# Kernel optimization log

Measured on AMD Instinct MI355X. Metric: run time of the kernel, lower is better.

Reference implementation:

```python
import jax, jax.numpy as jnp
import numpy as np

HEADS = 16
WINDOW = 256
D_MODEL = 1024


def _ln(x, g, b, eps=1e-5):
    m = jnp.mean(x, -1, keepdims=True)
    var = jnp.mean((x - m) ** 2, -1, keepdims=True)
    return (x - m) * jax.lax.rsqrt(var + eps) * g + b


def _proj(x, g, b, W, bias):
    # torch: nn.Sequential(LayerNorm(d), Linear(d, h))
    return _ln(x, g, b) @ W.T + bias


def _bucket(x, pad_value):
    # x: (..., L, d) -> (..., nb, window, d), seq padded to multiple of window with pad_value
    L = x.shape[-2]
    n = WINDOW * (-(-L // WINDOW))
    pads = [(0, 0)] * x.ndim
    pads[-2] = (0, n - L)
    x = jnp.pad(x, pads, constant_values=pad_value)
    return x.reshape(*x.shape[:-2], n // WINDOW, WINDOW, x.shape[-1])


def _unfold(x, pad_value):
    # x: (..., nb, w, d) -> (..., nb, 2w, d): previous bucket (pad_value for bucket 0) || current
    pads = [(0, 0)] * x.ndim
    pads[-3] = (1, 0)
    prev = jnp.pad(x, pads, constant_values=pad_value)[..., :-1, :, :]
    return jnp.concatenate([prev, x], axis=-2)


def _rotary(x):
    # lucidrains rotary_embedding_torch default: theta=10000, interleaved pairs, positions 0..S-1 along dim -2
    S, d = x.shape[-2], x.shape[-1]
    inv = 1.0 / (10000.0 ** (jnp.arange(0, d, 2, dtype=jnp.float32) / d))
    freqs = jnp.arange(S, dtype=jnp.float32)[:, None] * inv[None, :]  # (S, d/2)
    freqs = jnp.repeat(freqs, 2, axis=-1)  # (S, d)
    cos, sin = jnp.cos(freqs).astype(x.dtype), jnp.sin(freqs).astype(x.dtype)
    xp = x.reshape(*x.shape[:-1], d // 2, 2)
    xr = jnp.stack([-xp[..., 1], xp[..., 0]], axis=-1).reshape(x.shape)
    return x * cos + xr * sin


def _forward(q, k, v, cell,
             ln_q_w, ln_q_b, w_q, b_q,
             ln_k_w, ln_k_b, w_k, b_k,
             ln_v_w, ln_v_b, w_v, b_v,
             ln_o_w, ln_o_b, w_o, b_o):
    B, L, D = q.shape
    hd = D // HEADS

    def split_heads(x):  # (B, L, D) -> (B, H, L, hd)
        return x.reshape(B, L, HEADS, hd).transpose(0, 2, 1, 3)

    qh = split_heads(_proj(q, ln_q_w, ln_q_b, w_q, b_q))
    kh = split_heads(_proj(k, ln_k_w, ln_k_b, w_k, b_k))
    vh = split_heads(_proj(v, ln_v_w, ln_v_b, w_v, b_v))

    bq = _bucket(qh, -1.0)                 # (B, H, nb, w, hd)
    bk = _unfold(_bucket(kh, -1.0), -1.0)  # (B, H, nb, 2w, hd)
    bv = _unfold(_bucket(vh, -1.0), -1.0)

    nb = bq.shape[2]
    n = nb * WINDOW
    i = _bucket(jnp.arange(n, dtype=jnp.int32)[:, None], -1)   # (nb, w, 1)
    j = jnp.swapaxes(_unfold(i, -1), -1, -2)                    # (nb, 1, 2w)
    mask = (i >= j) & (j != -1)                                 # (nb, w, 2w) causal + left pad
    req = _bucket(cell, -1)                                     # (B, 1, nb, w, 1)
    rek = jnp.swapaxes(_unfold(req, -1), -1, -2)                # (B, 1, nb, 1, 2w)
    mask = mask & (req == rek)                                  # (B, 1, nb, w, 2w)

    bq = _rotary(bq)
    bk = _rotary(bk)

    p = jnp.einsum('bhnqd,bhnkd->bhnqk', bq, bk) / jnp.sqrt(jnp.asarray(hd, bq.dtype))
    p = jnp.where(mask, p, jnp.finfo(p.dtype).min)
    a = jax.nn.softmax(p, axis=-1)
    o = jnp.einsum('bhnqk,bhnkd->bhnqd', a, bv)   # (B, H, nb, w, hd)
    o = o.reshape(B, HEADS, n, hd)[:, :, :L]      # drop seq padding
    o = o.transpose(0, 2, 1, 3).reshape(B, L, D)  # merge heads
    return _proj(o, ln_o_w, ln_o_b, w_o, b_o)


def setup_inputs() -> dict:
    key = jax.random.key(0)
    ks = jax.random.split(key, 10)
    B, L, D = 2, 4096, D_MODEL
    inp = {
        'q': jax.random.normal(ks[0], (B, L, D), dtype=jnp.float32),
        'k': jax.random.normal(ks[1], (B, L, D), dtype=jnp.float32),
        'v': jax.random.normal(ks[2], (B, L, D), dtype=jnp.float32),
        'cell': jnp.sort(jax.random.randint(ks[3], (B, 1, L, 1), 0, 64, dtype=jnp.int32), axis=2),
    }
    for idx, name in enumerate(['q', 'k', 'v', 'o']):
        inp[f'ln_{name}_w'] = jnp.ones((D,), jnp.float32)
        inp[f'ln_{name}_b'] = jnp.zeros((D,), jnp.float32)
        inp[f'w_{name}'] = jax.random.normal(ks[4 + idx], (D, D), dtype=jnp.float32) * 0.02
        inp[f'b_{name}'] = jnp.zeros((D,), jnp.float32)
    return inp


def reference(q, k, v, cell,
              ln_q_w, ln_q_b, w_q, b_q,
              ln_k_w, ln_k_b, w_k, b_k,
              ln_v_w, ln_v_b, w_v, b_v,
              ln_o_w, ln_o_b, w_o, b_o):
    return _forward(q, k, v, cell,
                    ln_q_w, ln_q_b, w_q, b_q,
                    ln_k_w, ln_k_b, w_k, b_k,
                    ln_v_w, ln_v_b, w_v, b_v,
                    ln_o_w, ln_o_b, w_o, b_o)
```

## Files before the change

### kernel.cpp

```cpp
#include <hip/hip_runtime.h>

#define HEADS 16
#define HD 64
#define DM 1024
#define LSEQ 4096
#define NEGF (-1.0e30f)

typedef __attribute__((ext_vector_type(8))) short bf16x8;
typedef __attribute__((ext_vector_type(4))) float f32x4;
typedef unsigned short u16;

#define MFMA16(a, b, c) __builtin_amdgcn_mfma_f32_16x16x32_bf16((a), (b), (c), 0, 0, 0)

static __device__ __forceinline__ float b2f(u16 u) {
  union { float f; unsigned i; } t; t.i = ((unsigned)u) << 16; return t.f;
}
static __device__ __forceinline__ u16 f2b(float f) {
  union { float f; unsigned i; } t; t.f = f;
  unsigned r = t.i + 0x7fffu + ((t.i >> 16) & 1u);
  return (u16)(r >> 16);
}
static __device__ __forceinline__ ushort4 pk4(float4 v) {
  return make_ushort4(f2b(v.x), f2b(v.y), f2b(v.z), f2b(v.w));
}
static __device__ __forceinline__ void gload16(const void* g, void* l) {
  __builtin_amdgcn_global_load_lds((const __attribute__((address_space(1))) void*)g,
                                   (__attribute__((address_space(3))) void*)l, 16, 0, 0);
}

__global__ void rope_build(float* __restrict__ ropc, float* __restrict__ rops) {
  int p = blockIdx.x, d = threadIdx.x;
  int t2 = d & ~1;
  double inv = pow(10000.0, -(double)t2 / 64.0);
  double f = (double)p * inv;
  ropc[p * 64 + d] = (float)cos(f);
  rops[p * 64 + d] = (float)sin(f);
}

__global__ void cvtw(const float4* __restrict__ a, const float4* __restrict__ b,
                     const float4* __restrict__ c, const float4* __restrict__ d,
                     ushort4* __restrict__ out) {
  int i = blockIdx.x * blockDim.x + threadIdx.x;
  out[i]          = pk4(a[i]);
  out[i + 262144] = pk4(b[i]);
  out[i + 524288] = pk4(c[i]);
  out[i + 786432] = pk4(d[i]);
}

__global__ __launch_bounds__(256) void ln_qkv(
    const float4* __restrict__ q, const float4* __restrict__ k, const float4* __restrict__ v,
    const float* __restrict__ g0, const float* __restrict__ b0,
    const float* __restrict__ g1, const float* __restrict__ b1,
    const float* __restrict__ g2, const float* __restrict__ b2,
    ushort4* __restrict__ o0, ushort4* __restrict__ o1, ushort4* __restrict__ o2) {
  const int row = blockIdx.x, tid = threadIdx.x, sel = blockIdx.y;
  const float4* src = (sel == 0) ? q : (sel == 1) ? k : v;
  const float* gam = (sel == 0) ? g0 : (sel == 1) ? g1 : g2;
  const float* bet = (sel == 0) ? b0 : (sel == 1) ? b1 : b2;
  ushort4* dst = (sel == 0) ? o0 : (sel == 1) ? o1 : o2;

  float4 v4 = src[(size_t)row * 256 + tid];
  float s = v4.x + v4.y + v4.z + v4.w;
  float s2 = v4.x * v4.x + v4.y * v4.y + v4.z * v4.z + v4.w * v4.w;
#pragma unroll
  for (int d = 1; d < 64; d <<= 1) { s += __shfl_xor(s, d); s2 += __shfl_xor(s2, d); }
  __shared__ float ps[8];
  int lane = tid & 63, wave = tid >> 6;
  if (lane == 0) { ps[wave] = s; ps[4 + wave] = s2; }
  __syncthreads();
  float tot = ps[0] + ps[1] + ps[2] + ps[3];
  float tot2 = ps[4] + ps[5] + ps[6] + ps[7];
  float mean = tot * (1.f / 1024.f);
  float var = tot2 * (1.f / 1024.f) - mean * mean;
  float rstd = rsqrtf(var + 1e-5f);
  float4 gv = ((const float4*)gam)[tid];
  float4 bv = ((const float4*)bet)[tid];
  dst[(size_t)row * 256 + tid] = make_ushort4(
      f2b((v4.x - mean) * rstd * gv.x + bv.x), f2b((v4.y - mean) * rstd * gv.y + bv.y),
      f2b((v4.z - mean) * rstd * gv.z + bv.z), f2b((v4.w - mean) * rstd * gv.w + bv.w));
}

__global__ __launch_bounds__(256) void ln_rows(const ushort4* __restrict__ xin,
                                               const float* __restrict__ gam,
                                               const float* __restrict__ bet,
                                               ushort4* __restrict__ out) {
  int row = blockIdx.x, tid = threadIdx.x;
  ushort4 u = xin[(size_t)row * 256 + tid];
  float4 v;
  v.x = b2f(u.x); v.y = b2f(u.y); v.z = b2f(u.z); v.w = b2f(u.w);
  float s = v.x + v.y + v.z + v.w;
  float s2 = v.x * v.x + v.y * v.y + v.z * v.z + v.w * v.w;
#pragma unroll
  for (int d = 1; d < 64; d <<= 1) { s += __shfl_xor(s, d); s2 += __shfl_xor(s2, d); }
  __shared__ float ps[8];
  int lane = tid & 63, wave = tid >> 6;
  if (lane == 0) { ps[wave] = s; ps[4 + wave] = s2; }
  __syncthreads();
  float tot = ps[0] + ps[1] + ps[2] + ps[3];
  float tot2 = ps[4] + ps[5] + ps[6] + ps[7];
  float mean = tot * (1.f / 1024.f);
  float var = tot2 * (1.f / 1024.f) - mean * mean;
  float rstd = rsqrtf(var + 1e-5f);
  float4 gv = ((const float4*)gam)[tid];
  float4 bv = ((const float4*)bet)[tid];
  out[(size_t)row * 256 + tid] = make_ushort4(
      f2b((v.x - mean) * rstd * gv.x + bv.x), f2b((v.y - mean) * rstd * gv.y + bv.y),
      f2b((v.z - mean) * rstd * gv.z + bv.z), f2b((v.w - mean) * rstd * gv.w + bv.w));
}

__global__ __launch_bounds__(256, 3) void gemm_qkv(
    const u16* __restrict__ Aq, const u16* __restrict__ Ak, const u16* __restrict__ Av,
    const u16* __restrict__ wbf,
    const float* __restrict__ bq, const float* __restrict__ bk, const float* __restrict__ bv,
    const float* __restrict__ ropc, const float* __restrict__ rops,
    u16* __restrict__ qrot, u16* __restrict__ krA, u16* __restrict__ krB,
    u16* __restrict__ vTp) {
  __shared__ __align__(16) u16 Als[128 * 64];
  __shared__ __align__(16) u16 Bls[128 * 64];
  const int tid = threadIdx.x, lane = tid & 63, wave = tid >> 6;
  const int g = lane >> 4, ln15 = lane & 15;
  const int mode = blockIdx.y;
  const u16* A = (mode == 0) ? Aq : (mode == 1) ? Ak : Av;
  const u16* Bw = wbf + (size_t)mode * 1048576;
  const float* bias = (mode == 0) ? bq : (mode == 1) ? bk : bv;
  const int bid = blockIdx.x;
  const int xcd = bid & 7, idx = bid >> 3;
  const int row0 = (xcd * 8 + (idx >> 3)) * 128;
  const int col0 = (idx & 7) * 128;
  const int wm = (wave >> 1) * 64, wn = (wave & 1) * 64;
  const int K = 1024;
  f32x4 acc[4][4] = {};

  for (int k0 = 0; k0 < K; k0 += 64) {
#pragma unroll
    for (int i = 0; i < 4; ++i) {
      int ch = i * 4 + wave;
      int olin = ch * 1024 + lane * 16;
      int r = olin >> 7;
      int cel = ((olin ^ ((r & 7) << 4)) >> 1) & 63;
      gload16(A + (size_t)(row0 + r) * K + k0 + cel, (char*)Als + ch * 1024);
    }
#pragma unroll
    for (int i = 0; i < 4; ++i) {
      int ch = i * 4 + wave;
      int olin = ch * 1024 + lane * 16;
      int r = olin >> 7;
      int cel = ((olin ^ ((r & 7) << 4)) >> 1) & 63;
      gload16(Bw + (size_t)(col0 + r) * K + k0 + cel, (char*)Bls + ch * 1024);
    }
    __syncthreads();
#pragma unroll
    for (int ks = 0; ks < 2; ++ks) {
      bf16x8 af[4], bfv[4];
      int cb = (ks * 32 + g * 8) * 2;
#pragma unroll
      for (int mi = 0; mi < 4; ++mi) {
        int r = wm + mi * 16 + ln15;
        af[mi] = *(const bf16x8*)((const char*)Als + r * 128 + (cb ^ ((r & 7) << 4)));
      }
#pragma unroll
      for (int ni = 0; ni < 4; ++ni) {
        int r = wn + ni * 16 + ln15;
        bfv[ni] = *(const bf16x8*)((const char*)Bls + r * 128 + (cb ^ ((r & 7) << 4)));
      }
#pragma unroll
      for (int mi = 0; mi < 4; ++mi)
#pragma unroll
        for (int ni = 0; ni < 4; ++ni)
          acc[mi][ni] = MFMA16(af[mi], bfv[ni], acc[mi][ni]);
    }
    __syncthreads();
  }

#pragma unroll
  for (int mi = 0; mi < 4; ++mi)
#pragma unroll
    for (int ni = 0; ni < 4; ++ni)
#pragma unroll
      for (int r = 0; r < 4; ++r) {
        int row = row0 + wm + mi * 16 + g * 4 + r;
        int col = col0 + wn + ni * 16 + ln15;
        float val = acc[mi][ni][r] + bias[col];
        int bb = row >> 12, l = row & 4095, hh = col >> 6, d = col & 63;
        if (mode == 2) {
          vTp[(((size_t)bb * HEADS + hh) * HD + d) * LSEQ + l] = f2b(val);
        } else {
          if (mode == 0) val *= 0.125f;
          float oth = __shfl_xor(val, 1);
          int pB = l & 255;
          size_t oidx = (((size_t)bb * HEADS + hh) * LSEQ + l) * HD + d;
          if (mode == 0) {
            float cc = ropc[pB * 64 + d], ss = rops[pB * 64 + d];
            qrot[oidx] = f2b((d & 1) ? (val * cc + oth * ss) : (val * cc - oth * ss));
          } else {
            int pA = 256 + pB;
            float cA = ropc[pA * 64 + d], sA = rops[pA * 64 + d];
            krA[oidx] = f2b((d & 1) ? (val * cA + oth * sA) : (val * cA - oth * sA));
            float cB = ropc[pB * 64 + d], sB = rops[pB * 64 + d];
            krB[oidx] = f2b((d & 1) ? (val * cB + oth * sB) : (val * cB - oth * sB));
          }
        }
      }
}

__global__ __launch_bounds__(256, 3) void gemm_o(
    const u16* __restrict__ A, const u16* __restrict__ Bw, const float* __restrict__ bias,
    float* __restrict__ outf) {
  __shared__ __align__(16) u16 Als[128 * 64];
  __shared__ __align__(16) u16 Bls[128 * 64];
  const int tid = threadIdx.x, lane = tid & 63, wave = tid >> 6;
  const int g = lane >> 4, ln15 = lane & 15;
  const int bid = blockIdx.x;
  const int xcd = bid & 7, idx = bid >> 3;
  const int row0 = (xcd * 8 + (idx >> 3)) * 128;
  const int col0 = (idx & 7) * 128;
  const int wm = (wave >> 1) * 64, wn = (wave & 1) * 64;
  const int K = 1024, N = 1024;
  f32x4 acc[4][4] = {};

  for (int k0 = 0; k0 < K; k0 += 64) {
#pragma unroll
    for (int i = 0; i < 4; ++i) {
      int ch = i * 4 + wave;
      int olin = ch * 1024 + lane * 16;
      int r = olin >> 7;
      int cel = ((olin ^ ((r & 7) << 4)) >> 1) & 63;
      gload16(A + (size_t)(row0 + r) * K + k0 + cel, (char*)Als + ch * 1024);
    }
#pragma unroll
    for (int i = 0; i < 4; ++i) {
      int ch = i * 4 + wave;
      int olin = ch * 1024 + lane * 16;
      int r = olin >> 7;
      int cel = ((olin ^ ((r & 7) << 4)) >> 1) & 63;
      gload16(Bw + (size_t)(col0 + r) * K + k0 + cel, (char*)Bls + ch * 1024);
    }
    __syncthreads();
#pragma unroll
    for (int ks = 0; ks < 2; ++ks) {
      bf16x8 af[4], bfv[4];
      int cb = (ks * 32 + g * 8) * 2;
#pragma unroll
      for (int mi = 0; mi < 4; ++mi) {
        int r = wm + mi * 16 + ln15;
        af[mi] = *(const bf16x8*)((const char*)Als + r * 128 + (cb ^ ((r & 7) << 4)));
      }
#pragma unroll
      for (int ni = 0; ni < 4; ++ni) {
        int r = wn + ni * 16 + ln15;
        bfv[ni] = *(const bf16x8*)((const char*)Bls + r * 128 + (cb ^ ((r & 7) << 4)));
      }
#pragma unroll
      for (int mi = 0; mi < 4; ++mi)
#pragma unroll
        for (int ni = 0; ni < 4; ++ni)
          acc[mi][ni] = MFMA16(af[mi], bfv[ni], acc[mi][ni]);
    }
    __syncthreads();
  }

#pragma unroll
  for (int mi = 0; mi < 4; ++mi)
#pragma unroll
    for (int ni = 0; ni < 4; ++ni)
#pragma unroll
      for (int r = 0; r < 4; ++r) {
        int row = row0 + wm + mi * 16 + g * 4 + r;
        int col = col0 + wn + ni * 16 + ln15;
        outf[(size_t)row * N + col] = acc[mi][ni][r] + bias[col];
      }
}

__global__ __launch_bounds__(512, 2) void attn_kernel(
    const u16* __restrict__ qrot,
    const u16* __restrict__ krotA,
    const u16* __restrict__ krotB,
    const u16* __restrict__ vT,
    const int* __restrict__ cell,
    u16* __restrict__ o) {
  __shared__ __align__(16) u16 Kc[2][128 * 64];
  __shared__ __align__(16) u16 Pl[8 * 32 * 64];
  __shared__ int ci[256];
  __shared__ int cj[512];

  const int tid = threadIdx.x, lane = tid & 63, wave = tid >> 6;
  const int g = lane >> 4, ln15 = lane & 15;
  const int bucket = blockIdx.x & 15;
  const int h = (blockIdx.x >> 4) & 15;
  const int b = blockIdx.x >> 8;
  const int w0 = bucket * 256;
  const size_t base = (size_t)(b * HEADS + h) * LSEQ * HD;

  if (tid < 256) ci[tid] = cell[b * LSEQ + w0 + tid];
  {
    int gj = w0 - 256 + tid;
    cj[tid] = (gj >= 0) ? cell[b * LSEQ + gj] : (int)0x80000000;
  }

  bf16x8 qf[2][2];
#pragma unroll
  for (int mi = 0; mi < 2; ++mi)
#pragma unroll
    for (int ks = 0; ks < 2; ++ks)
      qf[mi][ks] = *(const bf16x8*)(qrot + base +
          (size_t)(w0 + wave * 32 + mi * 16 + ln15) * HD + ks * 32 + g * 8);

  f32x4 Oa[2][4] = {};
  float mrow[2][4], lrow[2][4];
#pragma unroll
  for (int a1 = 0; a1 < 2; ++a1)
#pragma unroll
    for (int a2 = 0; a2 < 4; ++a2) { mrow[a1][a2] = NEGF; lrow[a1][a2] = 0.f; }

#define STAGE_K(bi, s)                                                          \
  {                                                                             \
    const u16* ksrc_ = ((s) < 2) ? krotB : krotA;                               \
    int gj0_ = w0 - 256 + (s) * 128;                                            \
    _Pragma("unroll")                                                           \
    for (int i_ = 0; i_ < 2; ++i_) {                                            \
      int ch_ = i_ * 8 + wave;                                                  \
      int olin_ = ch_ * 1024 + lane * 16;                                       \
      int r_ = olin_ >> 7;                                                      \
      int cel_ = ((olin_ ^ ((r_ & 7) << 4)) >> 1) & 63;                         \
      gload16(ksrc_ + base + (size_t)(gj0_ + r_) * HD + cel_,                   \
              (char*)Kc[bi] + ch_ * 1024);                                      \
    }                                                                           \
  }

  const int s0 = (bucket == 0) ? 2 : 0;
  STAGE_K(0, s0);
  __syncthreads();

  const int crb_lo = ci[0], crb_hi = ci[255];
  const int crw_lo = ci[wave * 32], crw_hi = ci[wave * 32 + 31];

  for (int s = s0; s < 4; ++s) {
    const int cur = (s - s0) & 1;
    if (s + 1 < 4) {
      int k1 = (s + 1) * 2;
      bool need = false;
#pragma unroll
      for (int kk = 0; kk < 2; ++kk) {
        int clo = cj[(k1 + kk) * 64], chi = cj[(k1 + kk) * 64 + 63];
        need = need || !(chi < crb_lo || clo > crb_hi);
      }
      if (need) STAGE_K(cur ^ 1, s + 1);
    }

#pragma unroll
    for (int sub = 0; sub < 2; ++sub) {
      const int k = s * 2 + sub;
      if (k * 64 > wave * 32 + 287) continue;
      {
        int clo = cj[k * 64], chi = cj[k * 64 + 63];
        if (chi < crw_lo || clo > crw_hi) continue;
      }
      const int gj0 = w0 - 256 + k * 64;
      const int lr0 = sub * 64;

#pragma unroll
      for (int mi = 0; mi < 2; ++mi) {
        f32x4 sc[4] = {};
        __builtin_amdgcn_s_setprio(1);
#pragma unroll
        for (int ks = 0; ks < 2; ++ks) {
          int cb = (ks * 32 + g * 8) * 2;
#pragma unroll
          for (int ni = 0; ni < 4; ++ni) {
            int r = lr0 + ni * 16 + ln15;
            bf16x8 kf = *(const bf16x8*)((const char*)Kc[cur] + r * 128 + (cb ^ ((r & 7) << 4)));
            sc[ni] = MFMA16(qf[mi][ks], kf, sc[ni]);
          }
        }
        __builtin_amdgcn_s_setprio(0);
        float mx[4] = {NEGF, NEGF, NEGF, NEGF};
#pragma unroll
        for (int ni = 0; ni < 4; ++ni)
#pragma unroll
          for (int r = 0; r < 4; ++r) {
            int iloc = wave * 32 + mi * 16 + g * 4 + r;
            int p = k * 64 + ni * 16 + ln15;
            bool ok = (p <= iloc + 256) && (ci[iloc] == cj[p]);
            float sv = ok ? sc[ni][r] : NEGF;
            sc[ni][r] = sv;
            mx[r] = fmaxf(mx[r], sv);
          }
#pragma unroll
        for (int d = 1; d < 16; d <<= 1)
#pragma unroll
          for (int r = 0; r < 4; ++r) mx[r] = fmaxf(mx[r], __shfl_xor(mx[r], d));
        float rs[4] = {0.f, 0.f, 0.f, 0.f};
        bool big = false;
#pragma unroll
        for (int r = 0; r < 4; ++r) big = big || (mx[r] > mrow[mi][r] + 8.0f);
        if (__any(big)) {
#pragma unroll
          for (int r = 0; r < 4; ++r) {
            float mold = mrow[mi][r];
            float mnew = fmaxf(mold, mx[r]);
            float alpha = __expf(mold - mnew);
            mrow[mi][r] = mnew;
            lrow[mi][r] *= alpha;
#pragma unroll
            for (int nd = 0; nd < 4; ++nd) Oa[mi][nd][r] *= alpha;
          }
        }
#pragma unroll
        for (int ni = 0; ni < 4; ++ni)
#pragma unroll
          for (int r = 0; r < 4; ++r) {
            float sv = sc[ni][r];
            float p = (sv > NEGF * 0.5f) ? __expf(sv - mrow[mi][r]) : 0.f;
            rs[r] += p;
            int row = mi * 16 + g * 4 + r;
            int colb = (ni * 16 + ln15) * 2;
            *(u16*)((char*)Pl + wave * 4096 + row * 128 + (colb ^ ((row & 7) << 4))) = f2b(p);
          }
#pragma unroll
        for (int d = 1; d < 16; d <<= 1)
#pragma unroll
          for (int r = 0; r < 4; ++r) rs[r] += __shfl_xor(rs[r], d);
#pragma unroll
        for (int r = 0; r < 4; ++r) lrow[mi][r] += rs[r];
      }

#pragma unroll
      for (int jb = 0; jb < 2; ++jb) {
        bf16x8 pa[2], vb[4];
        int cb = (jb * 32 + g * 8) * 2;
#pragma unroll
        for (int mi = 0; mi < 2; ++mi) {
          int row = mi * 16 + ln15;
          pa[mi] = *(const bf16x8*)((const char*)Pl + wave * 4096 + row * 128 + (cb ^ ((row & 7) << 4)));
        }
#pragma unroll
        for (int nd = 0; nd < 4; ++nd) {
          int d = nd * 16 + ln15;
          int p0 = gj0 + jb * 32 + g * 8;
          vb[nd] = *(const bf16x8*)(vT + base + (size_t)d * LSEQ + p0);
        }
        __builtin_amdgcn_s_setprio(1);
#pragma unroll
        for (int mi = 0; mi < 2; ++mi)
#pragma unroll
          for (int nd = 0; nd < 4; ++nd) Oa[mi][nd] = MFMA16(pa[mi], vb[nd], Oa[mi][nd]);
        __builtin_amdgcn_s_setprio(0);
      }
    }

    __syncthreads();
  }

#pragma unroll
  for (int mi = 0; mi < 2; ++mi)
#pragma unroll
    for (int r = 0; r < 4; ++r) {
      float invl = 1.0f / lrow[mi][r];
      int gi = w0 + wave * 32 + mi * 16 + g * 4 + r;
      size_t ob = ((size_t)b * LSEQ + gi) * DM + h * HD;
#pragma unroll
      for (int nd = 0; nd < 4; ++nd) o[ob + nd * 16 + ln15] = f2b(Oa[mi][nd][r] * invl);
    }
#undef STAGE_K
}

extern "C" void kernel_launch(void* const* d_in, const int* in_sizes, int n_in,
                              void* d_out, int out_size, void* d_ws, size_t ws_size,
                              hipStream_t stream) {
  const float* q = (const float*)d_in[0];
  const float* k = (const float*)d_in[1];
  const float* v = (const float*)d_in[2];
  const int* cell = (const int*)d_in[3];
  const float* lnw[4] = {(const float*)d_in[4], (const float*)d_in[8], (const float*)d_in[12], (const float*)d_in[16]};
  const float* lnb[4] = {(const float*)d_in[5], (const float*)d_in[9], (const float*)d_in[13], (const float*)d_in[17]};
  const float* Wm[4]  = {(const float*)d_in[6], (const float*)d_in[10], (const float*)d_in[14], (const float*)d_in[18]};
  const float* bi[4]  = {(const float*)d_in[7], (const float*)d_in[11], (const float*)d_in[15], (const float*)d_in[19]};

  char* ws = (char*)d_ws;
  u16* xlnq  = (u16*)(ws);
  u16* wbf   = (u16*)(ws + 16777216);
  u16* qrot  = (u16*)(ws + 25165824);
  u16* krA   = (u16*)(ws + 41943040);
  u16* krB   = (u16*)(ws + 58720256);
  u16* vT    = (u16*)(ws + 75497472);
  u16* obuf  = (u16*)(ws + 92274688);
  float* ropc = (float*)(ws + 109051904);
  float* rops = (float*)(ws + 109182976);
  u16* xlnk = obuf;
  u16* xlnv = (u16*)d_out;

  cvtw<<<1024, 256, 0, stream>>>((const float4*)Wm[0], (const float4*)Wm[1],
                                 (const float4*)Wm[2], (const float4*)Wm[3], (ushort4*)wbf);
  rope_build<<<512, 64, 0, stream>>>(ropc, rops);

  dim3 lng(8192, 3);
  ln_qkv<<<lng, 256, 0, stream>>>((const float4*)q, (const float4*)k, (const float4*)v,
                                  lnw[0], lnb[0], lnw[1], lnb[1], lnw[2], lnb[2],
                                  (ushort4*)xlnq, (ushort4*)xlnk, (ushort4*)xlnv);
  dim3 gq(512, 3);
  gemm_qkv<<<gq, 256, 0, stream>>>(xlnq, xlnk, xlnv, wbf, bi[0], bi[1], bi[2],
                                   ropc, rops, qrot, krA, krB, vT);
  attn_kernel<<<512, 512, 0, stream>>>(qrot, krA, krB, vT, cell, obuf);
  ln_rows<<<8192, 256, 0, stream>>>((const ushort4*)obuf, lnw[3], lnb[3], (ushort4*)xlnq);
  gemm_o<<<512, 256, 0, stream>>>(xlnq, wbf + 3145728, bi[3], (float*)d_out);
}
```

Baseline: 214.7 us.

## Stage QKV GEMM epilogue through LDS and drop duplicate rotated K buffer

```diff
diff --git a/kernel.cpp b/kernel.cpp
--- a/kernel.cpp
+++ b/kernel.cpp
@@ -113,10 +113,10 @@
     const u16* __restrict__ wbf,
     const float* __restrict__ bq, const float* __restrict__ bk, const float* __restrict__ bv,
     const float* __restrict__ ropc, const float* __restrict__ rops,
-    u16* __restrict__ qrot, u16* __restrict__ krA, u16* __restrict__ krB,
-    u16* __restrict__ vTp) {
-  __shared__ __align__(16) u16 Als[128 * 64];
-  __shared__ __align__(16) u16 Bls[128 * 64];
+    u16* __restrict__ qrot, u16* __restrict__ krot, u16* __restrict__ vTp) {
+  __shared__ __align__(16) char smem[34816];
+  u16* Als = (u16*)smem;
+  u16* Bls = (u16*)(smem + 16384);
   const int tid = threadIdx.x, lane = tid & 63, wave = tid >> 6;
   const int g = lane >> 4, ln15 = lane & 15;
   const int mode = blockIdx.y;
@@ -172,35 +172,51 @@
     __syncthreads();
   }
 
+  u16* Cl = (u16*)smem;
 #pragma unroll
   for (int mi = 0; mi < 4; ++mi)
 #pragma unroll
     for (int ni = 0; ni < 4; ++ni)
 #pragma unroll
       for (int r = 0; r < 4; ++r) {
-        int row = row0 + wm + mi * 16 + g * 4 + r;
-        int col = col0 + wn + ni * 16 + ln15;
+        int rowc = wm + mi * 16 + g * 4 + r;
+        int colc = wn + ni * 16 + ln15;
+        int row = row0 + rowc, col = col0 + colc;
         float val = acc[mi][ni][r] + bias[col];
-        int bb = row >> 12, l = row & 4095, hh = col >> 6, d = col & 63;
         if (mode == 2) {
-          vTp[(((size_t)bb * HEADS + hh) * HD + d) * LSEQ + l] = f2b(val);
+          Cl[colc * 136 + rowc] = f2b(val);
         } else {
           if (mode == 0) val *= 0.125f;
           float oth = __shfl_xor(val, 1);
-          int pB = l & 255;
-          size_t oidx = (((size_t)bb * HEADS + hh) * LSEQ + l) * HD + d;
-          if (mode == 0) {
-            float cc = ropc[pB * 64 + d], ss = rops[pB * 64 + d];
-            qrot[oidx] = f2b((d & 1) ? (val * cc + oth * ss) : (val * cc - oth * ss));
-          } else {
-            int pA = 256 + pB;
-            float cA = ropc[pA * 64 + d], sA = rops[pA * 64 + d];
-            krA[oidx] = f2b((d & 1) ? (val * cA + oth * sA) : (val * cA - oth * sA));
-            float cB = ropc[pB * 64 + d], sB = rops[pB * 64 + d];
-            krB[oidx] = f2b((d & 1) ? (val * cB + oth * sB) : (val * cB - oth * sB));
-          }
+          int d = col & 63;
+          int pp = (row & 255) + ((mode == 1) ? 256 : 0);
+          float cc = ropc[pp * 64 + d], ss = rops[pp * 64 + d];
+          Cl[rowc * 136 + colc] = f2b((d & 1) ? (val * cc + oth * ss) : (val * cc - oth * ss));
         }
       }
+  __syncthreads();
+  if (mode == 2) {
+#pragma unroll
+    for (int i = 0; i < 8; ++i) {
+      int c2 = i * 256 + tid;
+      int dloc = c2 >> 4, lgrp = c2 & 15;
+      bf16x8 vv = *(const bf16x8*)(Cl + dloc * 136 + lgrp * 8);
+      int colg = col0 + dloc, hh = colg >> 6, d = colg & 63;
+      int l = row0 + lgrp * 8, bb = l >> 12, ll = l & 4095;
+      *(bf16x8*)(vTp + (((size_t)bb * HEADS + hh) * HD + d) * LSEQ + ll) = vv;
+    }
+  } else {
+    u16* dst = (mode == 0) ? qrot : krot;
+#pragma unroll
+    for (int i = 0; i < 8; ++i) {
+      int c2 = i * 256 + tid;
+      int rowc = c2 >> 4, cgrp = c2 & 15;
+      bf16x8 vv = *(const bf16x8*)(Cl + rowc * 136 + cgrp * 8);
+      int l = row0 + rowc, bb = l >> 12, ll = l & 4095;
+      int colg = col0 + cgrp * 8, hh = colg >> 6, d0 = colg & 63;
+      *(bf16x8*)(dst + (((size_t)bb * HEADS + hh) * LSEQ + ll) * HD + d0) = vv;
+    }
+  }
 }
 
 __global__ __launch_bounds__(256, 3) void gemm_o(
@@ -273,10 +289,10 @@
 
 __global__ __launch_bounds__(512, 2) void attn_kernel(
     const u16* __restrict__ qrot,
-    const u16* __restrict__ krotA,
-    const u16* __restrict__ krotB,
+    const u16* __restrict__ krot,
     const u16* __restrict__ vT,
     const int* __restrict__ cell,
+    const float* __restrict__ ropc, const float* __restrict__ rops,
     u16* __restrict__ o) {
   __shared__ __align__(16) u16 Kc[2][128 * 64];
   __shared__ __align__(16) u16 Pl[8 * 32 * 64];
@@ -305,6 +321,29 @@
       qf[mi][ks] = *(const bf16x8*)(qrot + base +
           (size_t)(w0 + wave * 32 + mi * 16 + ln15) * HD + ks * 32 + g * 8);
 
+  bf16x8 qfB[2][2];
+#pragma unroll
+  for (int ks = 0; ks < 2; ++ks) {
+    const int d0 = ks * 32 + g * 8;
+    float rc[8], rs8[8];
+#pragma unroll
+    for (int j = 0; j < 8; ++j) {
+      rc[j] = ropc[256 * 64 + d0 + j];
+      rs8[j] = rops[256 * 64 + d0 + j];
+    }
+#pragma unroll
+    for (int mi = 0; mi < 2; ++mi) {
+      bf16x8 s = qf[mi][ks], t;
+#pragma unroll
+      for (int j = 0; j < 8; j += 2) {
+        float e = b2f((u16)s[j]), od = b2f((u16)s[j + 1]);
+        t[j]     = (short)f2b(e * rc[j] - od * rs8[j]);
+        t[j + 1] = (short)f2b(e * rs8[j] + od * rc[j]);
+      }
+      qfB[mi][ks] = t;
+    }
+  }
+
   f32x4 Oa[2][4] = {};
   float mrow[2][4], lrow[2][4];
 #pragma unroll
@@ -314,7 +353,6 @@
 
 #define STAGE_K(bi, s)                                                          \
   {                                                                             \
-    const u16* ksrc_ = ((s) < 2) ? krotB : krotA;                               \
     int gj0_ = w0 - 256 + (s) * 128;                                            \
     _Pragma("unroll")                                                           \
     for (int i_ = 0; i_ < 2; ++i_) {                                            \
@@ -322,7 +360,7 @@
       int olin_ = ch_ * 1024 + lane * 16;                                       \
       int r_ = olin_ >> 7;                                                      \
       int cel_ = ((olin_ ^ ((r_ & 7) << 4)) >> 1) & 63;                         \
-      gload16(ksrc_ + base + (size_t)(gj0_ + r_) * HD + cel_,                   \
+      gload16(krot + base + (size_t)(gj0_ + r_) * HD + cel_,                    \
               (char*)Kc[bi] + ch_ * 1024);                                      \
     }                                                                           \
   }
@@ -357,6 +395,7 @@
       }
       const int gj0 = w0 - 256 + k * 64;
       const int lr0 = sub * 64;
+      const bool prevhalf = (k < 4);
 
 #pragma unroll
       for (int mi = 0; mi < 2; ++mi) {
@@ -365,11 +404,12 @@
 #pragma unroll
         for (int ks = 0; ks < 2; ++ks) {
           int cb = (ks * 32 + g * 8) * 2;
+          bf16x8 aq = prevhalf ? qfB[mi][ks] : qf[mi][ks];
 #pragma unroll
           for (int ni = 0; ni < 4; ++ni) {
             int r = lr0 + ni * 16 + ln15;
             bf16x8 kf = *(const bf16x8*)((const char*)Kc[cur] + r * 128 + (cb ^ ((r & 7) << 4)));
-            sc[ni] = MFMA16(qf[mi][ks], kf, sc[ni]);
+            sc[ni] = MFMA16(aq, kf, sc[ni]);
           }
         }
         __builtin_amdgcn_s_setprio(0);
@@ -480,8 +520,7 @@
   u16* xlnq  = (u16*)(ws);
   u16* wbf   = (u16*)(ws + 16777216);
   u16* qrot  = (u16*)(ws + 25165824);
-  u16* krA   = (u16*)(ws + 41943040);
-  u16* krB   = (u16*)(ws + 58720256);
+  u16* krot  = (u16*)(ws + 41943040);
   u16* vT    = (u16*)(ws + 75497472);
   u16* obuf  = (u16*)(ws + 92274688);
   float* ropc = (float*)(ws + 109051904);
@@ -499,8 +538,8 @@
                                   (ushort4*)xlnq, (ushort4*)xlnk, (ushort4*)xlnv);
   dim3 gq(512, 3);
   gemm_qkv<<<gq, 256, 0, stream>>>(xlnq, xlnk, xlnv, wbf, bi[0], bi[1], bi[2],
-                                   ropc, rops, qrot, krA, krB, vT);
-  attn_kernel<<<512, 512, 0, stream>>>(qrot, krA, krB, vT, cell, obuf);
+                                   ropc, rops, qrot, krot, vT);
+  attn_kernel<<<512, 512, 0, stream>>>(qrot, krot, vT, cell, ropc, rops, obuf);
   ln_rows<<<8192, 256, 0, stream>>>((const ushort4*)obuf, lnw[3], lnb[3], (ushort4*)xlnq);
   gemm_o<<<512, 256, 0, stream>>>(xlnq, wbf + 3145728, bi[3], (float*)d_out);
 }
```

Result: faster. 198.1 us (-7.7%).
